# Optimization experiments

Measured on AMD Instinct MI355X. Metric: run time of the kernel, lower is better.

## Reference

```python
import jax, jax.numpy as jnp
from jax import lax
import numpy as np

B, C, S, H, DH, DV, DW = 16, 256, 64, 8, 32, 32, 32  # batch, channels, input_size, heads, d_h, d_v, d_w


def _dwconv(x, w, b):
    # depthwise 3x3 conv, stride 1, pad 1. w: [C,1,3,3]
    y = lax.conv_general_dilated(x, w, (1, 1), ((1, 1), (1, 1)),
                                 dimension_numbers=('NCHW', 'OIHW', 'NCHW'),
                                 feature_group_count=x.shape[1])
    return y + b[None, :, None, None]


def _linear(x, w, b):
    # torch Linear: w [out,in]
    return x @ w.T + b


def setup_inputs() -> dict:
    key = jax.random.key(0)
    ks = jax.random.split(key, 26)
    n = lambda k, shape, s=0.02: jax.random.normal(k, shape, jnp.float32) * s
    conv = lambda k: n(k, (C, 1, 3, 3), 0.1)
    return {
        'x': jax.random.normal(ks[0], (B, C, S, S), jnp.float32),
        'dw_qh_w': conv(ks[1]), 'dw_qh_b': n(ks[2], (C,)),
        'fc_qh_w': n(ks[3], (H * DH, C)), 'fc_qh_b': n(ks[4], (H * DH,)),
        'dw_kh_w': conv(ks[5]), 'dw_kh_b': n(ks[6], (C,)),
        'fc_kh_w': n(ks[7], (H * DH, C)), 'fc_kh_b': n(ks[8], (H * DH,)),
        'Bh': n(ks[9], (1, H, S, S)),
        'dw_v_w': conv(ks[10]), 'dw_v_b': n(ks[11], (C,)),
        'fc_v_w': n(ks[12], (H * DV, C)), 'fc_v_b': n(ks[13], (H * DV,)),
        'dw_qw_w': conv(ks[14]), 'dw_qw_b': n(ks[15], (C,)),
        'fc_qw_w': n(ks[16], (H * DW, C)), 'fc_qw_b': n(ks[17], (H * DW,)),
        'dw_kw_w': conv(ks[18]), 'dw_kw_b': n(ks[19], (C,)),
        'fc_kw_w': n(ks[20], (H * DW, C)), 'fc_kw_b': n(ks[21], (H * DW,)),
        'Bw': n(ks[22], (1, H, S, S)),
        'fc_o_w': n(ks[23], (C, H * DV)), 'fc_o_b': n(ks[24], (C,)),
    }


def reference(x, dw_qh_w, dw_qh_b, fc_qh_w, fc_qh_b,
              dw_kh_w, dw_kh_b, fc_kh_w, fc_kh_b, Bh,
              dw_v_w, dw_v_b, fc_v_w, fc_v_b,
              dw_qw_w, dw_qw_b, fc_qw_w, fc_qw_b,
              dw_kw_w, dw_kw_b, fc_kw_w, fc_kw_b, Bw,
              fc_o_w, fc_o_b):
    b, c, h, w = x.shape
    sh = DH ** -0.5
    sw = DW ** -0.5

    # height-axis queries/keys: dwconv -> adaptive avg pool over width -> linear
    qh = _dwconv(x, dw_qh_w, dw_qh_b).mean(axis=3).transpose(0, 2, 1)  # [b,h,c]
    qh = _linear(qh, fc_qh_w, fc_qh_b).reshape(b, h, H, DH).transpose(0, 2, 1, 3)  # [b,H,h,dh]
    kh = _dwconv(x, dw_kh_w, dw_kh_b).mean(axis=3).transpose(0, 2, 1)
    kh = _linear(kh, fc_kh_w, fc_kh_b).reshape(b, h, H, DH).transpose(0, 2, 1, 3)
    attn_h = jax.nn.softmax(jnp.einsum('bhid,bhjd->bhij', qh, kh) * sh + Bh, axis=-1)  # [b,H,h,h]

    # values over full HxW grid
    v = _dwconv(x, dw_v_w, dw_v_b).reshape(b, c, h * w).transpose(0, 2, 1)  # [b,hw,c]
    v = _linear(v, fc_v_w, fc_v_b).reshape(b, h, w, H, DV).transpose(0, 3, 1, 2, 4)  # [b,H,h,w,dv]
    v = v.reshape(b, H, h, w * DV)

    # width-axis queries/keys: dwconv -> adaptive avg pool over height -> linear
    qw = _dwconv(x, dw_qw_w, dw_qw_b).mean(axis=2).transpose(0, 2, 1)  # [b,w,c]
    qw = _linear(qw, fc_qw_w, fc_qw_b).reshape(b, w, H, DW).transpose(0, 2, 1, 3)  # [b,H,w,dw]
    kw = _dwconv(x, dw_kw_w, dw_kw_b).mean(axis=2).transpose(0, 2, 1)
    kw = _linear(kw, fc_kw_w, fc_kw_b).reshape(b, w, H, DW).transpose(0, 2, 1, 3)
    attn_w = jax.nn.softmax(jnp.einsum('bhid,bhjd->bhij', qw, kw) * sw + Bw, axis=-1)  # [b,H,w,w]

    # dual axial mixing: height attention, then width attention
    r = jnp.matmul(attn_h, v)                                # [b,H,h,w*dv]
    r = r.reshape(b, H, h, w, DV).transpose(0, 1, 2, 4, 3)    # [b,H,h,dv,w]
    r = r.reshape(b, H, h * DV, w)
    r = jnp.matmul(r, attn_w)                                # [b,H,h*dv,w]
    r = r.reshape(b, H, h, DV, w).transpose(0, 2, 4, 1, 3)    # [b,h,w,H,dv]
    r = r.reshape(b, h * w, H * DV)
    out = _linear(r, fc_o_w, fc_o_b).reshape(b, C, h, w)      # faithful to torch .view
    return out
```

## Files before the change

### kernel.cpp

```cpp
#include <hip/hip_runtime.h>
#include <hip/hip_bf16.h>

typedef float f4v __attribute__((ext_vector_type(4)));
typedef short s8v __attribute__((ext_vector_type(8)));
typedef unsigned short u8v __attribute__((ext_vector_type(8)));

__device__ __forceinline__ float bf2f(ushort u) {
  union { unsigned int i; float f; } c; c.i = ((unsigned int)u) << 16;
  return c.f;
}
__device__ __forceinline__ ushort f2bf(float f) {
  union { ushort s; __hip_bfloat16 h; } c; c.h = __float2bfloat16(f);
  return c.s;
}

__global__ __launch_bounds__(256) void k_prep(const float* __restrict__ w0,
                                              const float* __restrict__ w1,
                                              const float* __restrict__ w2,
                                              const float* __restrict__ w3,
                                              const float* __restrict__ wv,
                                              const float* __restrict__ wo,
                                              ushort* __restrict__ whl,
                                              ushort* __restrict__ wbf) {
  int bx = blockIdx.x;
  int tid = threadIdx.x;
  if (bx < 1024) {
    int mat = bx >> 8;
    int i = (bx & 255) * 256 + tid;
    const float* p = mat == 0 ? w0 : mat == 1 ? w1 : mat == 2 ? w2 : w3;
    float f = p[i];
    ushort hi = f2bf(f);
    ushort lo = f2bf(f - bf2f(hi));
    whl[(size_t)mat * 131072 + i] = hi;
    whl[(size_t)mat * 131072 + 65536 + i] = lo;
  } else {
    int idx = (bx - 1024) * 256 + tid;
    const float* src = (idx >> 16) ? wo : wv;
    wbf[idx] = f2bf(src[idx & 65535]);
  }
}

__global__ __launch_bounds__(256) void k_conv(
    const float* __restrict__ x,
    const float* __restrict__ wqh, const float* __restrict__ bqh,
    const float* __restrict__ wkh, const float* __restrict__ bkh,
    const float* __restrict__ wv,  const float* __restrict__ bv,
    const float* __restrict__ wqw, const float* __restrict__ bqw,
    const float* __restrict__ wkw, const float* __restrict__ bkw,
    ushort* __restrict__ convV,
    float* __restrict__ qhm, float* __restrict__ khm,
    float* __restrict__ qwm, float* __restrict__ kwm) {
  __shared__ float xs[68 * 68];
  __shared__ float wl[5][9];
  __shared__ float bl[5];

  int bx = blockIdx.x;
  int b = bx >> 8;
  int c = bx & 255;
  int tid = threadIdx.x;
  int lane = tid & 63, wave = tid >> 6;

  const float* xp = x + (size_t)(b * 256 + c) * 4096;
#pragma unroll
  for (int i = 0; i < 4; i++) {
    int flat = tid + i * 256;
    int r = flat >> 4, c4 = (flat & 15) * 4;
    float4 v = *(const float4*)(xp + r * 64 + c4);
    *(float4*)&xs[(r + 1) * 68 + 4 + c4] = v;
  }
  if (tid < 72) { xs[tid] = 0.f; xs[65 * 68 + tid] = 0.f; }
  if (tid >= 72 && tid < 200) {
    int t = tid - 72;
    int pr = (t & 63) + 1, side = t >> 6;
    xs[pr * 68 + (side ? 68 : 3)] = 0.f;
  }
  if (tid >= 200 && tid < 245) {
    int t = tid - 200;
    int cw = t / 9, wi = t % 9;
    const float* wp = cw == 0 ? wqh : cw == 1 ? wkh : cw == 2 ? wv
                    : cw == 3 ? wqw : wkw;
    wl[cw][wi] = wp[c * 9 + wi];
  } else if (tid >= 245 && tid < 250) {
    int cw = tid - 245;
    const float* bp = cw == 0 ? bqh : cw == 1 ? bkh : cw == 2 ? bv
                    : cw == 3 ? bqw : bkw;
    bl[cw] = bp[c];
  }
  __syncthreads();

  {
    int w = lane;
    int h0 = wave * 16;
    float v0 = wl[2][0], v1 = wl[2][1], v2 = wl[2][2];
    float v3 = wl[2][3], v4 = wl[2][4], v5 = wl[2][5];
    float v6 = wl[2][6], v7 = wl[2][7], v8 = wl[2][8];
    float bvv = bl[2];
    float a00 = xs[h0 * 68 + 3 + w], a01 = xs[h0 * 68 + 4 + w],
          a02 = xs[h0 * 68 + 5 + w];
    float a10 = xs[(h0 + 1) * 68 + 3 + w], a11 = xs[(h0 + 1) * 68 + 4 + w],
          a12 = xs[(h0 + 1) * 68 + 5 + w];
    ushort* cp = convV + (size_t)(b * 256 + c) * 4096 + h0 * 64 + w;
#pragma unroll
    for (int i = 0; i < 16; i++) {
      int pr = h0 + i + 2;
      float a20 = xs[pr * 68 + 3 + w];
      float a21 = xs[pr * 68 + 4 + w];
      float a22 = xs[pr * 68 + 5 + w];
      float acc = bvv;
      acc += a00 * v0 + a01 * v1 + a02 * v2;
      acc += a10 * v3 + a11 * v4 + a12 * v5;
      acc += a20 * v6 + a21 * v7 + a22 * v8;
      cp[i * 64] = f2bf(acc);
      a00 = a10; a01 = a11; a02 = a12;
      a10 = a20; a11 = a21; a12 = a22;
    }
  }

  if (wave == 0) {
    float rs = 0.f, e0 = 0.f, e1 = 0.f;
    const float* rowp = &xs[(lane + 1) * 68 + 4];
#pragma unroll
    for (int i = 0; i < 16; i++) {
      float4 v = *(const float4*)(rowp + i * 4);
      rs += (v.x + v.y) + (v.z + v.w);
      if (i == 0) e0 = v.x;
      if (i == 15) e1 = v.w;
    }
    float rsP = __shfl(rs, lane - 1, 64); rsP = (lane == 0) ? 0.f : rsP;
    float rsN = __shfl(rs, lane + 1, 64); rsN = (lane == 63) ? 0.f : rsN;
    float e0P = __shfl(e0, lane - 1, 64); e0P = (lane == 0) ? 0.f : e0P;
    float e0N = __shfl(e0, lane + 1, 64); e0N = (lane == 63) ? 0.f : e0N;
    float e1P = __shfl(e1, lane - 1, 64); e1P = (lane == 0) ? 0.f : e1P;
    float e1N = __shfl(e1, lane + 1, 64); e1N = (lane == 63) ? 0.f : e1N;
    float RS[3] = {rsP, rs, rsN};
    float E0[3] = {e0P, e0, e0N};
    float E1[3] = {e1P, e1, e1N};
    float vq = 0.f, vk = 0.f;
#pragma unroll
    for (int ky = 0; ky < 3; ky++) {
      vq += (wl[0][ky * 3] + wl[0][ky * 3 + 1] + wl[0][ky * 3 + 2]) * RS[ky]
            - wl[0][ky * 3] * E1[ky] - wl[0][ky * 3 + 2] * E0[ky];
      vk += (wl[1][ky * 3] + wl[1][ky * 3 + 1] + wl[1][ky * 3 + 2]) * RS[ky]
            - wl[1][ky * 3] * E1[ky] - wl[1][ky * 3 + 2] * E0[ky];
    }
    qhm[(size_t)(b * 256 + c) * 64 + lane] = vq * (1.f / 64.f) + bl[0];
    khm[(size_t)(b * 256 + c) * 64 + lane] = vk * (1.f / 64.f) + bl[1];
  } else if (wave == 1) {
    float cs = 0.f, f0 = 0.f, f1 = 0.f;
#pragma unroll
    for (int r = 0; r < 64; r++) {
      float v = xs[(r + 1) * 68 + 4 + lane];
      cs += v;
      if (r == 0) f0 = v;
      if (r == 63) f1 = v;
    }
    float csP = __shfl(cs, lane - 1, 64); csP = (lane == 0) ? 0.f : csP;
    float csN = __shfl(cs, lane + 1, 64); csN = (lane == 63) ? 0.f : csN;
    float f0P = __shfl(f0, lane - 1, 64); f0P = (lane == 0) ? 0.f : f0P;
    float f0N = __shfl(f0, lane + 1, 64); f0N = (lane == 63) ? 0.f : f0N;
    float f1P = __shfl(f1, lane - 1, 64); f1P = (lane == 0) ? 0.f : f1P;
    float f1N = __shfl(f1, lane + 1, 64); f1N = (lane == 63) ? 0.f : f1N;
    float CS[3] = {csP, cs, csN};
    float F0[3] = {f0P, f0, f0N};
    float F1[3] = {f1P, f1, f1N};
    float vq = 0.f, vk = 0.f;
#pragma unroll
    for (int kx = 0; kx < 3; kx++) {
      vq += (wl[3][kx] + wl[3][3 + kx] + wl[3][6 + kx]) * CS[kx]
            - wl[3][kx] * F1[kx] - wl[3][6 + kx] * F0[kx];
      vk += (wl[4][kx] + wl[4][3 + kx] + wl[4][6 + kx]) * CS[kx]
            - wl[4][kx] * F1[kx] - wl[4][6 + kx] * F0[kx];
    }
    qwm[(size_t)(b * 256 + c) * 64 + lane] = vq * (1.f / 64.f) + bl[3];
    kwm[(size_t)(b * 256 + c) * 64 + lane] = vk * (1.f / 64.f) + bl[4];
  }
}

template <int OUT_BF16, int AT>
__global__ __launch_bounds__(256) void k_mm(const ushort* __restrict__ A,
                                            const ushort* __restrict__ W,
                                            const float* __restrict__ bias,
                                            void* __restrict__ out) {
  __shared__ __align__(16) ushort As[128 * 40];
  __shared__ __align__(16) ushort Bs[128 * 40];

  int m0 = blockIdx.x * 128;
  int n0 = blockIdx.y * 128;
  int tid = threadIdx.x;
  int lane = tid & 63, wave = tid >> 6;
  int wm = (wave & 1) * 64, wn = (wave >> 1) * 64;
  int tm = lane & 15, quad = lane >> 4;

  const ushort* Abase;
  if (AT) {
    Abase = A + (size_t)(m0 >> 12) * (256 * 4096) + (m0 & 4095);
  } else {
    Abase = A + (size_t)m0 * 256;
  }

  f4v acc[4][4] = {};

  for (int kc = 0; kc < 256; kc += 32) {
    __syncthreads();
    if (AT) {
      int kr2 = (tid & 15) * 2, mg = tid >> 4;
      u8v v0 = *(const u8v*)&Abase[(size_t)(kc + kr2) * 4096 + mg * 8];
      u8v v1 = *(const u8v*)&Abase[(size_t)(kc + kr2 + 1) * 4096 + mg * 8];
#pragma unroll
      for (int j = 0; j < 8; j++) {
        ushort pr[2] = {v0[j], v1[j]};
        *(uint*)&As[(mg * 8 + j) * 40 + kr2] = *(uint*)pr;
      }
#pragma unroll
      for (int h = 0; h < 2; h++) {
        int ch = tid + h * 256;
        int mr = ch >> 2, k8 = (ch & 3) * 8;
        *(float4*)&Bs[mr * 40 + k8] =
            *(const float4*)&W[(size_t)(n0 + mr) * 256 + kc + k8];
      }
    } else {
#pragma unroll
      for (int h = 0; h < 2; h++) {
        int ch = tid + h * 256;
        int mr = ch >> 2, k8 = (ch & 3) * 8;
        *(float4*)&As[mr * 40 + k8] =
            *(const float4*)&Abase[(size_t)mr * 256 + kc + k8];
        *(float4*)&Bs[mr * 40 + k8] =
            *(const float4*)&W[(size_t)(n0 + mr) * 256 + kc + k8];
      }
    }
    __syncthreads();

    s8v a[4], bfr[4];
#pragma unroll
    for (int mi = 0; mi < 4; mi++)
      a[mi] = *(const s8v*)&As[(wm + mi * 16 + tm) * 40 + quad * 8];
#pragma unroll
    for (int ni = 0; ni < 4; ni++)
      bfr[ni] = *(const s8v*)&Bs[(wn + ni * 16 + tm) * 40 + quad * 8];
#pragma unroll
    for (int mi = 0; mi < 4; mi++)
#pragma unroll
      for (int ni = 0; ni < 4; ni++)
        acc[mi][ni] = __builtin_amdgcn_mfma_f32_16x16x32_bf16(
            a[mi], bfr[ni], acc[mi][ni], 0, 0, 0);
  }

#pragma unroll
  for (int mi = 0; mi < 4; mi++) {
#pragma unroll
    for (int ni = 0; ni < 4; ni++) {
      int col = n0 + wn + ni * 16 + tm;
      float bv = bias[col];
#pragma unroll
      for (int r = 0; r < 4; r++) {
        int row = m0 + wm + mi * 16 + quad * 4 + r;
        float v = acc[mi][ni][r] + bv;
        if (OUT_BF16)
          ((ushort*)out)[(size_t)row * 256 + col] = f2bf(v);
        else
          ((float*)out)[(size_t)row * 256 + col] = v;
      }
    }
  }
}

__global__ __launch_bounds__(256) void k_gemm4(
    const float* __restrict__ s0, const float* __restrict__ s1,
    const float* __restrict__ s2, const float* __restrict__ s3,
    const ushort* __restrict__ whl,
    const float* __restrict__ b0, const float* __restrict__ b1,
    const float* __restrict__ b2, const float* __restrict__ b3,
    float* __restrict__ d0, float* __restrict__ d1,
    float* __restrict__ d2, float* __restrict__ d3) {
  __shared__ __align__(16) ushort Ah[64 * 68];
  __shared__ __align__(16) ushort Al[64 * 68];
  __shared__ __align__(16) ushort Wh[64 * 68];
  __shared__ __align__(16) ushort Wl[64 * 68];

  int z = blockIdx.z;
  const float* At = z == 0 ? s0 : z == 1 ? s1 : z == 2 ? s2 : s3;
  const ushort* Whp = whl + (size_t)z * 131072;
  const ushort* Wlp = Whp + 65536;
  const float* bias = z == 0 ? b0 : z == 1 ? b1 : z == 2 ? b2 : b3;
  float* Cout = z == 0 ? d0 : z == 1 ? d1 : z == 2 ? d2 : d3;

  int b = blockIdx.x;
  int n0 = blockIdx.y * 64;
  const float* Ab = At + (size_t)b * 256 * 64;

  int tid = threadIdx.x;
  int lane = tid & 63, wave = tid >> 6;
  int tm = lane & 15, quad = lane >> 4;
  int wm = (wave & 1) * 32, wn = (wave >> 1) * 32;

  f4v acc[2][2] = {};

  for (int kc = 0; kc < 256; kc += 64) {
    __syncthreads();
#pragma unroll
    for (int t2 = 0; t2 < 2; t2++) {
      int task = tid + t2 * 256;
      int mq = task & 15, kp = task >> 4;
      int k0 = kp * 2, m0 = mq * 4;
      float4 v0 = *(const float4*)&Ab[(size_t)(kc + k0) * 64 + m0];
      float4 v1 = *(const float4*)&Ab[(size_t)(kc + k0 + 1) * 64 + m0];
      float f0[4] = {v0.x, v0.y, v0.z, v0.w};
      float f1[4] = {v1.x, v1.y, v1.z, v1.w};
#pragma unroll
      for (int j = 0; j < 4; j++) {
        ushort h0 = f2bf(f0[j]), h1 = f2bf(f1[j]);
        ushort l0 = f2bf(f0[j] - bf2f(h0)), l1 = f2bf(f1[j] - bf2f(h1));
        ushort ph[2] = {h0, h1};
        ushort pl[2] = {l0, l1};
        *(uint*)&Ah[(m0 + j) * 68 + k0] = *(uint*)ph;
        *(uint*)&Al[(m0 + j) * 68 + k0] = *(uint*)pl;
      }
    }
#pragma unroll
    for (int t2 = 0; t2 < 2; t2++) {
      int task = tid + t2 * 256;
      int nr = task >> 3, k8 = (task & 7) * 8;
      *(u8v*)&Wh[nr * 68 + k8] =
          *(const u8v*)&Whp[(size_t)(n0 + nr) * 256 + kc + k8];
      *(u8v*)&Wl[nr * 68 + k8] =
          *(const u8v*)&Wlp[(size_t)(n0 + nr) * 256 + kc + k8];
    }
    __syncthreads();

#pragma unroll
    for (int ks = 0; ks < 64; ks += 32) {
      s8v ah[2], al[2], bh[2], bl[2];
#pragma unroll
      for (int mi = 0; mi < 2; mi++) {
        int idx = (wm + mi * 16 + tm) * 68 + ks + quad * 8;
        union { s8v v; unsigned long long u[2]; } th, tl;
        th.u[0] = *(const unsigned long long*)&Ah[idx];
        th.u[1] = *(const unsigned long long*)&Ah[idx + 4];
        tl.u[0] = *(const unsigned long long*)&Al[idx];
        tl.u[1] = *(const unsigned long long*)&Al[idx + 4];
        ah[mi] = th.v;
        al[mi] = tl.v;
      }
#pragma unroll
      for (int ni = 0; ni < 2; ni++) {
        int idx = (wn + ni * 16 + tm) * 68 + ks + quad * 8;
        union { s8v v; unsigned long long u[2]; } th, tl;
        th.u[0] = *(const unsigned long long*)&Wh[idx];
        th.u[1] = *(const unsigned long long*)&Wh[idx + 4];
        tl.u[0] = *(const unsigned long long*)&Wl[idx];
        tl.u[1] = *(const unsigned long long*)&Wl[idx + 4];
        bh[ni] = th.v;
        bl[ni] = tl.v;
      }
#pragma unroll
      for (int mi = 0; mi < 2; mi++)
#pragma unroll
        for (int ni = 0; ni < 2; ni++) {
          acc[mi][ni] = __builtin_amdgcn_mfma_f32_16x16x32_bf16(
              ah[mi], bh[ni], acc[mi][ni], 0, 0, 0);
          acc[mi][ni] = __builtin_amdgcn_mfma_f32_16x16x32_bf16(
              ah[mi], bl[ni], acc[mi][ni], 0, 0, 0);
          acc[mi][ni] = __builtin_amdgcn_mfma_f32_16x16x32_bf16(
              al[mi], bh[ni], acc[mi][ni], 0, 0, 0);
        }
    }
  }

#pragma unroll
  for (int mi = 0; mi < 2; mi++) {
#pragma unroll
    for (int ni = 0; ni < 2; ni++) {
      int n = n0 + wn + ni * 16 + tm;
      float bv = bias[n];
#pragma unroll
      for (int r = 0; r < 4; r++) {
        int m = b * 64 + wm + mi * 16 + quad * 4 + r;
        Cout[(size_t)m * 256 + n] = acc[mi][ni][r] + bv;
      }
    }
  }
}

__global__ __launch_bounds__(256) void k_attn(
    const float* __restrict__ qh, const float* __restrict__ kh,
    const float* __restrict__ Bh, float* __restrict__ ah,
    const float* __restrict__ qw, const float* __restrict__ kw,
    const float* __restrict__ Bw, float* __restrict__ aw, float scale) {
  __shared__ float qs[64 * 33];
  __shared__ float ks[64 * 33];

  int bx = blockIdx.x;
  int setw = bx >> 7;
  int rem = bx & 127;
  int hd = rem & 7, b = rem >> 3;
  int tid = threadIdx.x;
  int wave = tid >> 6, lane = tid & 63;

  const float* q = setw ? qw : qh;
  const float* k = setw ? kw : kh;
  const float* Bb = setw ? Bw : Bh;
  float* attn = setw ? aw : ah;

#pragma unroll
  for (int it = 0; it < 8; it++) {
    int f = tid + it * 256;
    int j = f >> 5, d = f & 31;
    size_t src = (size_t)(b * 64 + j) * 256 + hd * 32 + d;
    qs[j * 33 + d] = q[src];
    ks[j * 33 + d] = k[src];
  }
  __syncthreads();

  const float* Bp = Bb + (size_t)(hd * 64) * 64;
  float* ap = attn + (size_t)((b * 8 + hd) * 64) * 64;
  int j = lane;
  for (int ig = 0; ig < 16; ig++) {
    int i = ig * 4 + wave;
    float dot = 0.f;
#pragma unroll
    for (int d = 0; d < 32; d++) dot += qs[i * 33 + d] * ks[j * 33 + d];
    float logit = dot * scale + Bp[i * 64 + j];
    float mx = logit;
#pragma unroll
    for (int off = 32; off > 0; off >>= 1)
      mx = fmaxf(mx, __shfl_xor(mx, off, 64));
    float e = __expf(logit - mx);
    float sum = e;
#pragma unroll
    for (int off = 32; off > 0; off >>= 1) sum += __shfl_xor(sum, off, 64);
    ap[i * 64 + j] = e / sum;
  }
}

__global__ __launch_bounds__(256) void k_av(const float* __restrict__ attn,
                                            const ushort* __restrict__ vlin,
                                            ushort* __restrict__ r1) {
  __shared__ __align__(16) ushort Ah[64 * 68];
  __shared__ __align__(16) ushort Al[64 * 68];
  __shared__ __align__(16) ushort Bt[256 * 68];

  int bx = blockIdx.x;
  int nt = bx & 7, hd = (bx >> 3) & 7, b = bx >> 6;
  int n0 = nt * 256;
  int tid = threadIdx.x;
  int lane = tid & 63, wave = tid >> 6;

  const float* ap = attn + (size_t)(b * 8 + hd) * 4096;
  {
    int i = tid >> 2;
    int j0 = (tid & 3) * 16;
#pragma unroll
    for (int p = 0; p < 4; p++) {
      float4 v = *(const float4*)&ap[i * 64 + j0 + p * 4];
      float f_[4] = {v.x, v.y, v.z, v.w};
      ushort ph[4], pl[4];
#pragma unroll
      for (int q = 0; q < 4; q++) {
        ph[q] = f2bf(f_[q]);
        pl[q] = f2bf(f_[q] - bf2f(ph[q]));
      }
      *(uint2*)&Ah[i * 68 + j0 + p * 4] = *(uint2*)ph;
      *(uint2*)&Al[i * 68 + j0 + p * 4] = *(uint2*)pl;
    }
  }
  {
#pragma unroll
    for (int p = 0; p < 4; p++) {
      int task = tid + p * 256;
      int jp = task & 31;
      int cc = task >> 5;
      int j = jp * 2;
      int c = cc * 8;
      int gcol = n0 + c;
      int w = gcol >> 5, dv = gcol & 31;
      const ushort* vp =
          &vlin[(size_t)(b * 4096 + j * 64 + w) * 256 + hd * 32 + dv];
      u8v v0 = *(const u8v*)vp;
      u8v v1 = *(const u8v*)(vp + 64 * 256);
#pragma unroll
      for (int q = 0; q < 8; q++) {
        ushort pr[2] = {(ushort)v0[q], (ushort)v1[q]};
        *(uint*)&Bt[(c + q) * 68 + j] = *(uint*)pr;
      }
    }
  }
  __syncthreads();

  int tm = lane & 15, quad = lane >> 4;
  int wn = wave * 64;
  f4v acc[4][4] = {};
#pragma unroll
  for (int kc = 0; kc < 64; kc += 32) {
    s8v ah_[4], al_[4], bb[4];
#pragma unroll
    for (int mi = 0; mi < 4; mi++) {
      int idx = (mi * 16 + tm) * 68 + kc + quad * 8;
      union { s8v v; unsigned long long u[2]; } th, tl;
      th.u[0] = *(const unsigned long long*)&Ah[idx];
      th.u[1] = *(const unsigned long long*)&Ah[idx + 4];
      tl.u[0] = *(const unsigned long long*)&Al[idx];
      tl.u[1] = *(const unsigned long long*)&Al[idx + 4];
      ah_[mi] = th.v;
      al_[mi] = tl.v;
    }
#pragma unroll
    for (int ni = 0; ni < 4; ni++) {
      int idx = (wn + ni * 16 + tm) * 68 + kc + quad * 8;
      union { s8v v; unsigned long long u[2]; } tb;
      tb.u[0] = *(const unsigned long long*)&Bt[idx];
      tb.u[1] = *(const unsigned long long*)&Bt[idx + 4];
      bb[ni] = tb.v;
    }
#pragma unroll
    for (int mi = 0; mi < 4; mi++)
#pragma unroll
      for (int ni = 0; ni < 4; ni++) {
        acc[mi][ni] = __builtin_amdgcn_mfma_f32_16x16x32_bf16(
            ah_[mi], bb[ni], acc[mi][ni], 0, 0, 0);
        acc[mi][ni] = __builtin_amdgcn_mfma_f32_16x16x32_bf16(
            al_[mi], bb[ni], acc[mi][ni], 0, 0, 0);
      }
  }

  ushort* rp = r1 + (size_t)(b * 8 + hd) * 64 * 2048;
#pragma unroll
  for (int mi = 0; mi < 4; mi++) {
#pragma unroll
    for (int ni = 0; ni < 4; ni++) {
      int col = n0 + wn + ni * 16 + tm;
#pragma unroll
      for (int r = 0; r < 4; r++) {
        int row = mi * 16 + quad * 4 + r;
        rp[(size_t)row * 2048 + col] = f2bf(acc[mi][ni][r]);
      }
    }
  }
}

__global__ __launch_bounds__(256) void k_rw(const ushort* __restrict__ r1,
                                            const float* __restrict__ attnw,
                                            ushort* __restrict__ yT) {
  __shared__ __align__(16) ushort As[8 * 2180];
  __shared__ __align__(16) ushort Wh[64 * 68];
  __shared__ __align__(16) ushort Wl[64 * 68];

  int bx = blockIdx.x;
  int ht = bx & 7, hd = (bx >> 3) & 7, b = bx >> 6;
  int tid = threadIdx.x;
  int lane = tid & 63, wave = tid >> 6;

  {
    int h = tid >> 5;
    int t = tid & 31;
    const ushort* rp =
        r1 + (size_t)((b * 8 + hd) * 64 + ht * 8 + h) * 2048;
#pragma unroll
    for (int i = 0; i < 4; i++) {
      int chunk = t + 32 * i;
      int w = (chunk >> 2) * 2;
      int dv0 = (chunk & 3) * 8;
      u8v v0 = *(const u8v*)&rp[w * 32 + dv0];
      u8v v1 = *(const u8v*)&rp[(w + 1) * 32 + dv0];
#pragma unroll
      for (int j = 0; j < 8; j++) {
        ushort pr[2] = {(ushort)v0[j], (ushort)v1[j]};
        *(uint*)&As[h * 2180 + (dv0 + j) * 68 + w] = *(uint*)pr;
      }
    }
  }
  {
    const float* ap = attnw + (size_t)(b * 8 + hd) * 4096;
#pragma unroll
    for (int p = 0; p < 4; p++) {
      int w = (tid >> 4) + p * 16;
      int wq = (tid & 15) * 4;
      float4 v = *(const float4*)&ap[w * 64 + wq];
      float f_[4] = {v.x, v.y, v.z, v.w};
#pragma unroll
      for (int j = 0; j < 4; j++) {
        ushort hi = f2bf(f_[j]);
        Wh[(wq + j) * 68 + w] = hi;
        Wl[(wq + j) * 68 + w] = f2bf(f_[j] - bf2f(hi));
      }
    }
  }
  __syncthreads();

  int tm = lane & 15, quad = lane >> 4;
  int h0 = wave * 2;
  f4v acc[4][4] = {};
#pragma unroll
  for (int kc = 0; kc < 64; kc += 32) {
    s8v a[4], bh[4], bl[4];
#pragma unroll
    for (int mi = 0; mi < 4; mi++) {
      int h = h0 + (mi >> 1);
      int dv = (mi & 1) * 16 + tm;
      int idx = h * 2180 + dv * 68 + kc + quad * 8;
      union { s8v v; unsigned long long u[2]; } t_;
      t_.u[0] = *(const unsigned long long*)&As[idx];
      t_.u[1] = *(const unsigned long long*)&As[idx + 4];
      a[mi] = t_.v;
    }
#pragma unroll
    for (int ni = 0; ni < 4; ni++) {
      int idx = (ni * 16 + tm) * 68 + kc + quad * 8;
      union { s8v v; unsigned long long u[2]; } th, tl;
      th.u[0] = *(const unsigned long long*)&Wh[idx];
      th.u[1] = *(const unsigned long long*)&Wh[idx + 4];
      tl.u[0] = *(const unsigned long long*)&Wl[idx];
      tl.u[1] = *(const unsigned long long*)&Wl[idx + 4];
      bh[ni] = th.v;
      bl[ni] = tl.v;
    }
#pragma unroll
    for (int mi = 0; mi < 4; mi++)
#pragma unroll
      for (int ni = 0; ni < 4; ni++) {
        acc[mi][ni] = __builtin_amdgcn_mfma_f32_16x16x32_bf16(
            a[mi], bh[ni], acc[mi][ni], 0, 0, 0);
        acc[mi][ni] = __builtin_amdgcn_mfma_f32_16x16x32_bf16(
            a[mi], bl[ni], acc[mi][ni], 0, 0, 0);
      }
  }

#pragma unroll
  for (int mi = 0; mi < 4; mi++) {
    int h = ht * 8 + h0 + (mi >> 1);
    int dv0 = (mi & 1) * 16 + quad * 4;
#pragma unroll
    for (int ni = 0; ni < 4; ni++) {
      int wp = ni * 16 + tm;
      ushort pk[4];
#pragma unroll
      for (int r = 0; r < 4; r++) pk[r] = f2bf(acc[mi][ni][r]);
      *(uint2*)&yT[(size_t)(b * 4096 + h * 64 + wp) * 256 + hd * 32 + dv0] =
          *(uint2*)pk;
    }
  }
}

extern "C" void kernel_launch(void* const* d_in, const int* in_sizes, int n_in,
                              void* d_out, int out_size, void* d_ws,
                              size_t ws_size, hipStream_t stream) {
  const float* x      = (const float*)d_in[0];
  const float* dwqh_w = (const float*)d_in[1];
  const float* dwqh_b = (const float*)d_in[2];
  const float* fcqh_w = (const float*)d_in[3];
  const float* fcqh_b = (const float*)d_in[4];
  const float* dwkh_w = (const float*)d_in[5];
  const float* dwkh_b = (const float*)d_in[6];
  const float* fckh_w = (const float*)d_in[7];
  const float* fckh_b = (const float*)d_in[8];
  const float* Bh     = (const float*)d_in[9];
  const float* dwv_w  = (const float*)d_in[10];
  const float* dwv_b  = (const float*)d_in[11];
  const float* fcv_w  = (const float*)d_in[12];
  const float* fcv_b  = (const float*)d_in[13];
  const float* dwqw_w = (const float*)d_in[14];
  const float* dwqw_b = (const float*)d_in[15];
  const float* fcqw_w = (const float*)d_in[16];
  const float* fcqw_b = (const float*)d_in[17];
  const float* dwkw_w = (const float*)d_in[18];
  const float* dwkw_b = (const float*)d_in[19];
  const float* fckw_w = (const float*)d_in[20];
  const float* fckw_b = (const float*)d_in[21];
  const float* Bw     = (const float*)d_in[22];
  const float* fco_w  = (const float*)d_in[23];
  const float* fco_b  = (const float*)d_in[24];

  char* base = (char*)d_ws;
  ushort* P1 = (ushort*)(base);
  ushort* P2 = (ushort*)(base + 33554432);
  ushort* P3 = (ushort*)(base + 67108864);
  ushort* whl  = (ushort*)(base + 100663296);
  ushort* wv_bf = (ushort*)(base + 101711872);
  float* qhm = (float*)(base + 101974016);
  float* khm = qhm + 262144;
  float* qwm = khm + 262144;
  float* kwm = qwm + 262144;
  float* qhl = kwm + 262144;
  float* khl = qhl + 262144;
  float* qwl = khl + 262144;
  float* kwl = qwl + 262144;
  float* ah  = kwl + 262144;
  float* awt = ah + 524288;
  if (ws_size < 115000000ull) return;

  const float scale = 0.17677669529663687f;

  k_prep<<<1536, 256, 0, stream>>>(fcqh_w, fckh_w, fcqw_w, fckw_w, fcv_w,
                                   fco_w, whl, wv_bf);
  k_conv<<<4096, 256, 0, stream>>>(x, dwqh_w, dwqh_b, dwkh_w, dwkh_b, dwv_w,
                                   dwv_b, dwqw_w, dwqw_b, dwkw_w, dwkw_b, P1,
                                   qhm, khm, qwm, kwm);
  k_gemm4<<<dim3(16, 4, 4), 256, 0, stream>>>(qhm, khm, qwm, kwm, whl, fcqh_b,
                                              fckh_b, fcqw_b, fckw_b, qhl, khl,
                                              qwl, kwl);
  k_attn<<<256, 256, 0, stream>>>(qhl, khl, Bh, ah, qwl, kwl, Bw, awt, scale);
  k_mm<1, 1><<<dim3(512, 2), 256, 0, stream>>>(P1, wv_bf, fcv_b, P3);
  k_av<<<1024, 256, 0, stream>>>(ah, P3, P1);
  k_rw<<<1024, 256, 0, stream>>>(P1, awt, P2);
  k_mm<0, 0><<<dim3(512, 2), 256, 0, stream>>>(P2, wv_bf + 65536, fco_b, d_out);
}
```

Before: 281.5 us.

## Fold weight prep into conv kernel and use direct global-to-LDS loads with XOR swizzle

The separate weight-conversion kernel is merged into the depthwise conv kernel as extra blocks, which removes one launch and lets the two overlap. The GEMM kernel now stages tiles with global_load_lds (direct global-to-LDS 16-byte loads) into an unpadded 32-wide LDS layout. Padding is replaced by an XOR swizzle on the 8-element slot to avoid bank conflicts, and the MFMA fragment reads are updated to match. This cuts register staging and LDS footprint, but it depends on the swizzle and the per-wave contiguous LDS destination layout being correct.

```diff
diff --git a/kernel.cpp b/kernel.cpp
--- a/kernel.cpp
+++ b/kernel.cpp
@@ -13,31 +13,10 @@
   union { ushort s; __hip_bfloat16 h; } c; c.h = __float2bfloat16(f);
   return c.s;
 }
-
-__global__ __launch_bounds__(256) void k_prep(const float* __restrict__ w0,
-                                              const float* __restrict__ w1,
-                                              const float* __restrict__ w2,
-                                              const float* __restrict__ w3,
-                                              const float* __restrict__ wv,
-                                              const float* __restrict__ wo,
-                                              ushort* __restrict__ whl,
-                                              ushort* __restrict__ wbf) {
-  int bx = blockIdx.x;
-  int tid = threadIdx.x;
-  if (bx < 1024) {
-    int mat = bx >> 8;
-    int i = (bx & 255) * 256 + tid;
-    const float* p = mat == 0 ? w0 : mat == 1 ? w1 : mat == 2 ? w2 : w3;
-    float f = p[i];
-    ushort hi = f2bf(f);
-    ushort lo = f2bf(f - bf2f(hi));
-    whl[(size_t)mat * 131072 + i] = hi;
-    whl[(size_t)mat * 131072 + 65536 + i] = lo;
-  } else {
-    int idx = (bx - 1024) * 256 + tid;
-    const float* src = (idx >> 16) ? wo : wv;
-    wbf[idx] = f2bf(src[idx & 65535]);
-  }
+__device__ __forceinline__ void gload16(const ushort* g, ushort* l) {
+  __builtin_amdgcn_global_load_lds(
+      (const __attribute__((address_space(1))) unsigned int*)g,
+      (__attribute__((address_space(3))) unsigned int*)l, 16, 0, 0);
 }
 
 __global__ __launch_bounds__(256) void k_conv(
@@ -47,6 +26,10 @@
     const float* __restrict__ wv,  const float* __restrict__ bv,
     const float* __restrict__ wqw, const float* __restrict__ bqw,
     const float* __restrict__ wkw, const float* __restrict__ bkw,
+    const float* __restrict__ fq0, const float* __restrict__ fq1,
+    const float* __restrict__ fq2, const float* __restrict__ fq3,
+    const float* __restrict__ fwv, const float* __restrict__ fwo,
+    ushort* __restrict__ whl, ushort* __restrict__ wbf,
     ushort* __restrict__ convV,
     float* __restrict__ qhm, float* __restrict__ khm,
     float* __restrict__ qwm, float* __restrict__ kwm) {
@@ -55,9 +38,29 @@
   __shared__ float bl[5];
 
   int bx = blockIdx.x;
+  int tid = threadIdx.x;
+
+  if (bx >= 4096) {
+    int pb = bx - 4096;
+    if (pb < 1024) {
+      int mat = pb >> 8;
+      int i = (pb & 255) * 256 + tid;
+      const float* p = mat == 0 ? fq0 : mat == 1 ? fq1 : mat == 2 ? fq2 : fq3;
+      float f = p[i];
+      ushort hi = f2bf(f);
+      ushort lo = f2bf(f - bf2f(hi));
+      whl[(size_t)mat * 131072 + i] = hi;
+      whl[(size_t)mat * 131072 + 65536 + i] = lo;
+    } else {
+      int idx = (pb - 1024) * 256 + tid;
+      const float* src = (idx >> 16) ? fwo : fwv;
+      wbf[idx] = f2bf(src[idx & 65535]);
+    }
+    return;
+  }
+
   int b = bx >> 8;
   int c = bx & 255;
-  int tid = threadIdx.x;
   int lane = tid & 63, wave = tid >> 6;
 
   const float* xp = x + (size_t)(b * 256 + c) * 4096;
@@ -181,8 +184,8 @@
                                             const ushort* __restrict__ W,
                                             const float* __restrict__ bias,
                                             void* __restrict__ out) {
-  __shared__ __align__(16) ushort As[128 * 40];
-  __shared__ __align__(16) ushort Bs[128 * 40];
+  __shared__ __align__(16) ushort As[128 * 32];
+  __shared__ __align__(16) ushort Bs[128 * 32];
 
   int m0 = blockIdx.x * 128;
   int n0 = blockIdx.y * 128;
@@ -190,6 +193,9 @@
   int lane = tid & 63, wave = tid >> 6;
   int wm = (wave & 1) * 64, wn = (wave >> 1) * 64;
   int tm = lane & 15, quad = lane >> 4;
+  int xorv = (tm ^ (tm >> 2)) & 3;
+  int srow = lane >> 2;
+  int slot = lane & 3;
 
   const ushort* Abase;
   if (AT) {
@@ -206,27 +212,32 @@
       int kr2 = (tid & 15) * 2, mg = tid >> 4;
       u8v v0 = *(const u8v*)&Abase[(size_t)(kc + kr2) * 4096 + mg * 8];
       u8v v1 = *(const u8v*)&Abase[(size_t)(kc + kr2 + 1) * 4096 + mg * 8];
+      int sl0 = kr2 >> 3, k7 = kr2 & 7;
 #pragma unroll
       for (int j = 0; j < 8; j++) {
+        int row = mg * 8 + j;
+        int xr = (row ^ (row >> 2)) & 3;
         ushort pr[2] = {v0[j], v1[j]};
-        *(uint*)&As[(mg * 8 + j) * 40 + kr2] = *(uint*)pr;
-      }
-#pragma unroll
-      for (int h = 0; h < 2; h++) {
-        int ch = tid + h * 256;
-        int mr = ch >> 2, k8 = (ch & 3) * 8;
-        *(float4*)&Bs[mr * 40 + k8] =
-            *(const float4*)&W[(size_t)(n0 + mr) * 256 + kc + k8];
+        *(uint*)&As[row * 32 + (sl0 ^ xr) * 8 + k7] = *(uint*)pr;
+      }
+#pragma unroll
+      for (int it = 0; it < 2; it++) {
+        int rb = wave * 16 + it * 64;
+        int row = rb + srow;
+        int xr = (row ^ (row >> 2)) & 3;
+        gload16(&W[(size_t)(n0 + row) * 256 + kc + (slot ^ xr) * 8],
+                &Bs[rb * 32]);
       }
     } else {
 #pragma unroll
-      for (int h = 0; h < 2; h++) {
-        int ch = tid + h * 256;
-        int mr = ch >> 2, k8 = (ch & 3) * 8;
-        *(float4*)&As[mr * 40 + k8] =
-            *(const float4*)&Abase[(size_t)mr * 256 + kc + k8];
-        *(float4*)&Bs[mr * 40 + k8] =
-            *(const float4*)&W[(size_t)(n0 + mr) * 256 + kc + k8];
+      for (int it = 0; it < 2; it++) {
+        int rb = wave * 16 + it * 64;
+        int row = rb + srow;
+        int xr = (row ^ (row >> 2)) & 3;
+        gload16(&Abase[(size_t)row * 256 + kc + (slot ^ xr) * 8],
+                &As[rb * 32]);
+        gload16(&W[(size_t)(n0 + row) * 256 + kc + (slot ^ xr) * 8],
+                &Bs[rb * 32]);
       }
     }
     __syncthreads();
@@ -234,10 +245,10 @@
     s8v a[4], bfr[4];
 #pragma unroll
     for (int mi = 0; mi < 4; mi++)
-      a[mi] = *(const s8v*)&As[(wm + mi * 16 + tm) * 40 + quad * 8];
+      a[mi] = *(const s8v*)&As[(wm + mi * 16 + tm) * 32 + (quad ^ xorv) * 8];
 #pragma unroll
     for (int ni = 0; ni < 4; ni++)
-      bfr[ni] = *(const s8v*)&Bs[(wn + ni * 16 + tm) * 40 + quad * 8];
+      bfr[ni] = *(const s8v*)&Bs[(wn + ni * 16 + tm) * 32 + (quad ^ xorv) * 8];
 #pragma unroll
     for (int mi = 0; mi < 4; mi++)
 #pragma unroll
@@ -690,10 +701,10 @@
 
   const float scale = 0.17677669529663687f;
 
-  k_prep<<<1536, 256, 0, stream>>>(fcqh_w, fckh_w, fcqw_w, fckw_w, fcv_w,
-                                   fco_w, whl, wv_bf);
-  k_conv<<<4096, 256, 0, stream>>>(x, dwqh_w, dwqh_b, dwkh_w, dwkh_b, dwv_w,
-                                   dwv_b, dwqw_w, dwqw_b, dwkw_w, dwkw_b, P1,
+  k_conv<<<5632, 256, 0, stream>>>(x, dwqh_w, dwqh_b, dwkh_w, dwkh_b, dwv_w,
+                                   dwv_b, dwqw_w, dwqw_b, dwkw_w, dwkw_b,
+                                   fcqh_w, fckh_w, fcqw_w, fckw_w, fcv_w,
+                                   fco_w, whl, wv_bf, P1,
                                    qhm, khm, qwm, kwm);
   k_gemm4<<<dim3(16, 4, 4), 256, 0, stream>>>(qhm, khm, qwm, kwm, whl, fcqh_b,
                                               fckh_b, fcqw_b, fckw_b, qhl, khl,
```

Measured after the change: 277.5 us. Within noise of the previous version (-1.4%).
